# Performance work log

Measured on AMD Instinct MI355X. Metric: run time of the kernel, lower is better.

The kernel has to match this reference:

```python
import jax, jax.numpy as jnp
import numpy as np

B, L, IN, H, T = 512, 16, 128, 1024, 64


def setup_inputs() -> dict:
    key = jax.random.key(0)
    ks = jax.random.split(key, 11)
    k = 1.0 / np.sqrt(H)  # torch default init scale
    u = lambda kk, shape: jax.random.uniform(kk, shape, jnp.float32, -k, k)
    return {
        "x": jax.random.normal(ks[0], (B, L, IN), jnp.float32),
        "W_ih0": u(ks[1], (4 * H, IN)),
        "W_hh0": u(ks[2], (4 * H, H)),
        "b_ih0": u(ks[3], (4 * H,)),
        "b_hh0": u(ks[4], (4 * H,)),
        "W_ih1": u(ks[5], (4 * H, H)),
        "W_hh1": u(ks[6], (4 * H, H)),
        "b_ih1": u(ks[7], (4 * H,)),
        "b_hh1": u(ks[8], (4 * H,)),
        "W_out": u(ks[9], (IN, H)),
        "b_out": u(ks[10], (IN,)),
        "t": T,
    }


def _cell(xt, h, c, W_ih, W_hh, b_ih, b_hh):
    # PyTorch LSTM cell; gate order i, f, g, o
    g = xt @ W_ih.T + h @ W_hh.T + (b_ih + b_hh)
    i, f, gg, o = jnp.split(g, 4, axis=-1)
    c = jax.nn.sigmoid(f) * c + jax.nn.sigmoid(i) * jnp.tanh(gg)
    h = jax.nn.sigmoid(o) * jnp.tanh(c)
    return h, c


def reference(x, W_ih0, W_hh0, b_ih0, b_hh0, W_ih1, W_hh1, b_ih1, b_hh1,
              W_out, b_out, t):
    layers = ((W_ih0, W_hh0, b_ih0, b_hh0), (W_ih1, W_hh1, b_ih1, b_hh1))
    Bn = x.shape[0]
    Hn = W_hh0.shape[1]

    def stack_step(state, xt):
        new_state = []
        inp = xt
        for (h, c), p in zip(state, layers):
            h, c = _cell(inp, h, c, *p)
            new_state.append((h, c))
            inp = h
        return tuple(new_state), inp  # inp = top-layer hidden [B, H]

    z = jnp.zeros((Bn, Hn), x.dtype)
    state0 = tuple((z, z) for _ in layers)

    # prompt phase: process x over time, keep final state and last top hidden
    state, tops = jax.lax.scan(stack_step, state0, x.transpose(1, 0, 2))
    x_last = x[:, -1] + (tops[-1] @ W_out.T + b_out)  # [B, IN]

    def gen_step(carry, _):
        st, xl = carry
        st, htop = stack_step(st, xl)
        xl = xl + (htop @ W_out.T + b_out)
        return (st, xl), xl

    (_, _), gen = jax.lax.scan(gen_step, (state, x_last), None, length=t - 1)

    out = jnp.concatenate(
        [x, x_last[:, None, :], gen.transpose(1, 0, 2)], axis=1
    )  # [B, L + t, IN]
    return out
```

## Files before the change

### kernel.cpp

```cpp
#include <hip/hip_runtime.h>

#define B_    512
#define L_    16
#define IN_   128
#define H_    1024
#define T_    64
#define OUTROW 10240

#define LDC   1040
#define LDXL  144
#define RSTRIDE 67
#define RSZ   (64 * RSTRIDE)

#define KH_X  64
#define KH_H  32
#define KH_XL 4
#define KH_W0 36
#define KH_W1 64
#define KH_WO 32

typedef __attribute__((ext_vector_type(8))) short bf8;
typedef __attribute__((ext_vector_type(4))) float f4;
typedef __attribute__((ext_vector_type(4))) unsigned short us4;
typedef unsigned short u16;
typedef unsigned int   u32;

#define MFMA16(a, b, c) __builtin_amdgcn_mfma_f32_16x16x32_bf16(a, b, c, 0, 0, 0)

__device__ __forceinline__ u16 f2bf(float f) {
    u32 u = __builtin_bit_cast(u32, f);
    u32 r = (u + 0x7fffu + ((u >> 16) & 1u)) >> 16;
    return (u16)r;
}
__device__ __forceinline__ float sigm(float x) { return 1.f / (1.f + __expf(-x)); }
__device__ __forceinline__ float tanh_f(float x) {
    float ax = fabsf(x);
    float e = __expf(-2.f * ax);
    float t = (1.f - e) / (1.f + e);
    return x < 0.f ? -t : t;
}
__device__ __forceinline__ bf8 ld8(const u16* p) { return *(const bf8*)p; }

__device__ __forceinline__ size_t swz(int kh_stride, int row, int k) {
    return ((size_t)(row >> 4) * kh_stride + (k >> 5)) * 512
           + ((k & 31) >> 3) * 128 + (row & 15) * 8 + (k & 7);
}

#define MFMAP(AS, BS)                                                       \
  do {                                                                      \
    _Pragma("unroll")                                                       \
    for (int g_ = 0; g_ < 4; ++g_)                                          \
      _Pragma("unroll")                                                     \
      for (int t_ = 0; t_ < 4; ++t_)                                        \
        acc[g_][t_] = MFMA16(AS[g_], BS[t_], acc[g_][t_]);                  \
  } while (0)

#define LOADP_CELL(AS, BS, PH)                                              \
  do {                                                                      \
    const int kt_ = ws + (((PH) >> 1) << 2);                                \
    const int s_  = (PH) & 1;                                               \
    const bool ix_ = kt_ < nk1;                                             \
    const int oA_ = (((ix_ ? kt_ : kt_ - nk1) << 1) + s_) * 512;            \
    const int oB_ = ((kt_ << 1) + s_) * 512;                                \
    _Pragma("unroll")                                                       \
    for (int g_ = 0; g_ < 4; ++g_)                                          \
      AS[g_] = ld8((ix_ ? apx[g_] : aph[g_]) + oA_);                        \
    _Pragma("unroll")                                                       \
    for (int t_ = 0; t_ < 4; ++t_) BS[t_] = ld8(bp[t_] + oB_);              \
  } while (0)

__device__ __forceinline__ void cell_body(int bid,
    const u16* __restrict__ pA0, int kh0, int nk1,
    const u16* __restrict__ pA1, int kh1, int nk2,
    const u16* __restrict__ pB, int khB,
    const float* __restrict__ bias, float* __restrict__ Cst,
    u16* __restrict__ Hdst, float* __restrict__ red)
{
    const int tn = (bid & 7) * 8 + ((bid >> 3) & 7);
    const int tm = bid >> 6;
    const int tid = threadIdx.x;
    const int lane = tid & 63, ws = tid >> 6;
    const int l15 = lane & 15, qd = lane >> 4, q4 = qd * 4;

    const int erow = ws * 16 + l15;
    const int grow = tm * 64 + erow;
    const int colb = tn * 16 + q4;
    const f4 cold = *(const f4*)&Cst[(size_t)grow * LDC + colb];

    f4 acc[4][4];
#pragma unroll
    for (int i = 0; i < 4; ++i)
#pragma unroll
        for (int j = 0; j < 4; ++j) acc[i][j] = (f4)(0.f);

    const u16* bp[4];
#pragma unroll
    for (int t = 0; t < 4; ++t)
        bp[t] = pB + (size_t)(tn * 4 + t) * khB * 512 + lane * 8;
    const u16* apx[4];
    const u16* aph[4];
#pragma unroll
    for (int g = 0; g < 4; ++g) {
        apx[g] = pA0 + (size_t)(tm * 4 + g) * kh0 * 512 + lane * 8;
        aph[g] = pA1 + (size_t)(tm * 4 + g) * kh1 * 512 + lane * 8;
    }

    const int nk  = nk1 + nk2;
    const int myn = (nk - ws + 3) >> 2;
    const int nph = myn * 2;

    bf8 A0[4], B0[4], A1[4], B1[4], A2[4], B2[4], A3[4], B3[4];
    LOADP_CELL(A0, B0, 0);
    LOADP_CELL(A1, B1, 1);
    LOADP_CELL(A2, B2, 2);
    int ph = 0;
    for (; ph + 4 <= nph; ph += 4) {
        LOADP_CELL(A3, B3, ph + 3);
        MFMAP(A0, B0);
        if (ph + 4 < nph) LOADP_CELL(A0, B0, ph + 4);
        MFMAP(A1, B1);
        if (ph + 5 < nph) LOADP_CELL(A1, B1, ph + 5);
        MFMAP(A2, B2);
        if (ph + 6 < nph) LOADP_CELL(A2, B2, ph + 6);
        MFMAP(A3, B3);
    }
    if (ph < nph) {
        MFMAP(A0, B0);
        MFMAP(A1, B1);
    }

#pragma unroll
    for (int rg = 0; rg < 4; ++rg)
#pragma unroll
        for (int t = 0; t < 4; ++t)
#pragma unroll
            for (int r = 0; r < 4; ++r)
                red[ws * RSZ + (rg * 16 + q4 + r) * RSTRIDE + t * 16 + l15] = acc[rg][t][r];
    __syncthreads();

    f4 gs[4];
#pragma unroll
    for (int G = 0; G < 4; ++G) {
        f4 s;
#pragma unroll
        for (int j = 0; j < 4; ++j) {
            const int cidx = erow * RSTRIDE + G * 16 + q4 + j;
            s[j] = red[0 * RSZ + cidx] + red[1 * RSZ + cidx]
                 + red[2 * RSZ + cidx] + red[3 * RSZ + cidx];
        }
        gs[G] = s + *(const f4*)&bias[tn * 64 + G * 16 + q4];
    }
    f4 cn; us4 h4;
#pragma unroll
    for (int j = 0; j < 4; ++j) {
        const float I  = sigm(gs[0][j]);
        const float F  = sigm(gs[1][j]);
        const float Gg = tanh_f(gs[2][j]);
        const float O  = sigm(gs[3][j]);
        cn[j] = F * cold[j] + I * Gg;
        h4[j] = f2bf(O * tanh_f(cn[j]));
    }
    *(f4*)&Cst[(size_t)grow * LDC + colb] = cn;
    *(us4*)&Hdst[swz(KH_H, grow, colb)] = h4;
}

__global__ __launch_bounds__(256, 2) void cell_gemm(
    const u16* __restrict__ pA0, int kh0, int nk1,
    const u16* __restrict__ pA1, int kh1, int nk2,
    const u16* __restrict__ pB, int khB,
    const float* __restrict__ bias, float* __restrict__ Cst, u16* __restrict__ Hdst)
{
    __shared__ float red[4 * RSZ];
    cell_body(blockIdx.x, pA0, kh0, nk1, pA1, kh1, nk2, pB, khB, bias, Cst, Hdst, red);
}

__global__ __launch_bounds__(256, 2) void pair_k(
    const u16* __restrict__ A0a, int kh0a, int nk1a,
    const u16* __restrict__ A1a, int kh1a, int nk2a,
    const u16* __restrict__ Ba, int khBa,
    const float* __restrict__ ba, float* __restrict__ Ca, u16* __restrict__ Ha,
    const u16* __restrict__ A0b, int kh0b, int nk1b,
    const u16* __restrict__ A1b, int kh1b, int nk2b,
    const u16* __restrict__ Bb, int khBb,
    const float* __restrict__ bb, float* __restrict__ Cb, u16* __restrict__ Hb)
{
    __shared__ float red[4 * RSZ];
    if (blockIdx.x < 512)
        cell_body(blockIdx.x, A0a, kh0a, nk1a, A1a, kh1a, nk2a, Ba, khBa, ba, Ca, Ha, red);
    else
        cell_body(blockIdx.x - 512, A0b, kh0b, nk1b, A1b, kh1b, nk2b, Bb, khBb, bb, Cb, Hb, red);
}

__global__ __launch_bounds__(256, 2) void proj64_k(
    const u16* __restrict__ pH1, const u16* __restrict__ pWo,
    const float* __restrict__ bout_,
    const float* __restrict__ xin, int ldxin,
    float* __restrict__ XL, u16* __restrict__ XLbf,
    float* __restrict__ dout, int slot)
{
    __shared__ float red[4 * RSZ];
    const int pb = blockIdx.x;
    const int tm = pb >> 3, cg = pb & 7;
    const int tid = threadIdx.x;
    const int lane = tid & 63, ws = tid >> 6;
    const int l15 = lane & 15, qd = lane >> 4;

    const u16* ap[4];
#pragma unroll
    for (int g = 0; g < 4; ++g)
        ap[g] = pH1 + (size_t)(tm * 4 + g) * (KH_H * 512) + lane * 8;
    const u16* bp = pWo + (size_t)cg * (KH_WO * 512) + lane * 8;

    f4 acc[4];
#pragma unroll
    for (int g = 0; g < 4; ++g) acc[g] = (f4)(0.f);

    for (int m = 0; m < 4; ++m) {
#pragma unroll
        for (int sh = 0; sh < 2; ++sh) {
            const int o = (((ws + m * 4) << 1) + sh) * 512;
            const bf8 Bv = ld8(bp + o);
#pragma unroll
            for (int g = 0; g < 4; ++g)
                acc[g] = MFMA16(ld8(ap[g] + o), Bv, acc[g]);
        }
    }

#pragma unroll
    for (int g = 0; g < 4; ++g)
#pragma unroll
        for (int r = 0; r < 4; ++r)
            red[ws * RSZ + (g * 16 + qd * 4 + r) * RSTRIDE + l15] = acc[g][r];
    __syncthreads();

    const int row = tid >> 2, c4 = (tid & 3) * 4;
    const int col = cg * 16 + c4;
    const int grow = tm * 64 + row;
    f4 s;
#pragma unroll
    for (int j = 0; j < 4; ++j) {
        const int cidx = row * RSTRIDE + c4 + j;
        s[j] = red[0 * RSZ + cidx] + red[1 * RSZ + cidx]
             + red[2 * RSZ + cidx] + red[3 * RSZ + cidx];
    }
    const f4 v = *(const f4*)&xin[(size_t)grow * ldxin + col] + s
                 + *(const f4*)&bout_[col];
    *(f4*)&XL[(size_t)grow * LDXL + col] = v;
    us4 b;
#pragma unroll
    for (int j = 0; j < 4; ++j) b[j] = f2bf(v[j]);
    *(us4*)&XLbf[swz(KH_XL, grow, col)] = b;
    *(f4*)&dout[(size_t)grow * OUTROW + slot * IN_ + col] = v;
}

__global__ void conv_w(const float* Wih0, const float* Whh0, const float* bih0, const float* bhh0,
                       const float* Wih1, const float* Whh1, const float* bih1, const float* bhh1,
                       const float* Wout,
                       u16* W0c, float* b0p, u16* W1c, float* b1p, u16* Woutb)
{
    const int bid = blockIdx.x, t = threadIdx.x;
    const int lane = t >> 2;
    const int l15 = lane & 15, qd = lane >> 4;
    const int j0 = (t & 3) * 2;
    const int c0_ = qd * 8 + j0;

    if (bid < 9216) {
        const int rg = bid / 36, kh = bid - rg * 36;
        const int p = rg * 16 + l15;
        const int rem = p & 63, G = rem >> 4, u = (p >> 6) * 16 + (rem & 15);
        const int src = G * H_ + u;
        float e0, e1;
        if (kh < 4) {
            e0 = Wih0[(size_t)src * IN_ + kh * 32 + c0_];
            e1 = Wih0[(size_t)src * IN_ + kh * 32 + c0_ + 1];
        } else {
            e0 = Whh0[(size_t)src * H_ + (kh - 4) * 32 + c0_];
            e1 = Whh0[(size_t)src * H_ + (kh - 4) * 32 + c0_ + 1];
        }
        ((u32*)W0c)[(size_t)bid * 256 + t] = (u32)f2bf(e0) | ((u32)f2bf(e1) << 16);
        if (kh == 0 && qd == 0 && j0 == 0) b0p[p] = bih0[src] + bhh0[src];
    } else if (bid < 25600) {
        const int x = bid - 9216;
        const int rg = x >> 6, kh = x & 63;
        const int p = rg * 16 + l15;
        const int rem = p & 63, G = rem >> 4, u = (p >> 6) * 16 + (rem & 15);
        const int src = G * H_ + u;
        float e0, e1;
        if (kh < 32) {
            e0 = Wih1[(size_t)src * H_ + kh * 32 + c0_];
            e1 = Wih1[(size_t)src * H_ + kh * 32 + c0_ + 1];
        } else {
            e0 = Whh1[(size_t)src * H_ + (kh - 32) * 32 + c0_];
            e1 = Whh1[(size_t)src * H_ + (kh - 32) * 32 + c0_ + 1];
        }
        ((u32*)W1c)[(size_t)x * 256 + t] = (u32)f2bf(e0) | ((u32)f2bf(e1) << 16);
        if (kh == 0 && qd == 0 && j0 == 0) b1p[p] = bih1[src] + bhh1[src];
    } else {
        const int x = bid - 25600;
        const int rg = x >> 5, kh = x & 31;
        const int r = rg * 16 + l15;
        const float e0 = Wout[(size_t)r * H_ + kh * 32 + c0_];
        const float e1 = Wout[(size_t)r * H_ + kh * 32 + c0_ + 1];
        ((u32*)Woutb)[(size_t)x * 256 + t] = (u32)f2bf(e0) | ((u32)f2bf(e1) << 16);
    }
}

__global__ void setup_k(const float* __restrict__ x, u16* __restrict__ Xb,
                        u16* H0, u16* H1, float* c0, float* c1,
                        float* __restrict__ dout)
{
    const int i = blockIdx.x * 256 + threadIdx.x;
    const float v = x[i];
    const int r = i >> 11, col = i & 2047;
    Xb[swz(KH_X, r, col)] = f2bf(v);
    dout[(size_t)r * OUTROW + col] = v;
    if (i < B_ * H_) {
        H0[i] = 0; H1[i] = 0;
        const int rr = i >> 10, cc = i & 1023;
        c0[(size_t)rr * LDC + cc] = 0.f; c1[(size_t)rr * LDC + cc] = 0.f;
    }
}

extern "C" void kernel_launch(void* const* d_in, const int* in_sizes, int n_in,
                              void* d_out, int out_size, void* d_ws, size_t ws_size,
                              hipStream_t stream)
{
    const float* x    = (const float*)d_in[0];
    const float* Wih0 = (const float*)d_in[1];
    const float* Whh0 = (const float*)d_in[2];
    const float* bih0 = (const float*)d_in[3];
    const float* bhh0 = (const float*)d_in[4];
    const float* Wih1 = (const float*)d_in[5];
    const float* Whh1 = (const float*)d_in[6];
    const float* bih1 = (const float*)d_in[7];
    const float* bhh1 = (const float*)d_in[8];
    const float* Wout = (const float*)d_in[9];
    const float* bout = (const float*)d_in[10];
    float* dout = (float*)d_out;

    char* ws = (char*)d_ws;
    size_t off = 0;
    auto alloc = [&](size_t bytes) -> char* {
        char* p = ws + off; off += (bytes + 255) & ~(size_t)255; return p;
    };
    u16*  W0c   = (u16*)alloc((size_t)9216 * 1024);
    u16*  W1c   = (u16*)alloc((size_t)16384 * 1024);
    u16*  Woutb = (u16*)alloc((size_t)256 * 1024);
    float* b0p  = (float*)alloc(4096 * 4);
    float* b1p  = (float*)alloc(4096 * 4);
    u16*  Xb    = (u16*)alloc((size_t)2048 * 1024);
    u16*  H0b[2]; H0b[0] = (u16*)alloc((size_t)1024 * 1024); H0b[1] = (u16*)alloc((size_t)1024 * 1024);
    u16*  H1b[2]; H1b[0] = (u16*)alloc((size_t)1024 * 1024); H1b[1] = (u16*)alloc((size_t)1024 * 1024);
    float* c0   = (float*)alloc((size_t)B_ * LDC * 4);
    float* c1   = (float*)alloc((size_t)B_ * LDC * 4);
    float* XL   = (float*)alloc((size_t)B_ * LDXL * 4);
    u16*  XLbf  = (u16*)alloc((size_t)128 * 1024);

    conv_w<<<25856, 256, 0, stream>>>(Wih0, Whh0, bih0, bhh0,
                                      Wih1, Whh1, bih1, bhh1, Wout,
                                      W0c, b0p, W1c, b1p, Woutb);
    setup_k<<<4096, 256, 0, stream>>>(x, Xb, H0b[0], H1b[0], c0, c1, dout);

    int p = 0;
    cell_gemm<<<512, 256, 0, stream>>>(Xb, KH_X, 2, H0b[0], KH_H, 16,
                                       W0c, KH_W0, b0p, c0, H0b[1]);
    for (int g = 0; g < 15; ++g) {
        pair_k<<<1024, 256, 0, stream>>>(
            H0b[1 - p], KH_H, 16, H1b[p], KH_H, 16, W1c, KH_W1, b1p, c1, H1b[1 - p],
            Xb + (size_t)(g + 1) * 2048, KH_X, 2, H0b[1 - p], KH_H, 16,
            W0c, KH_W0, b0p, c0, H0b[p]);
        p ^= 1;
    }
    cell_gemm<<<512, 256, 0, stream>>>(H0b[0], KH_H, 16, H1b[1], KH_H, 16,
                                       W1c, KH_W1, b1p, c1, H1b[0]);
    proj64_k<<<64, 256, 0, stream>>>(H1b[0], Woutb, bout,
                                     x + 15 * IN_, L_ * IN_, XL, XLbf, dout, 16);

    p = 0;
    for (int g = 16; g < 79; ++g) {
        cell_gemm<<<512, 256, 0, stream>>>(XLbf, KH_XL, 2, H0b[p], KH_H, 16,
                                           W0c, KH_W0, b0p, c0, H0b[1 - p]);
        cell_gemm<<<512, 256, 0, stream>>>(H0b[1 - p], KH_H, 16, H1b[p], KH_H, 16,
                                           W1c, KH_W1, b1p, c1, H1b[1 - p]);
        const int s = g - 15;
        proj64_k<<<64, 256, 0, stream>>>(H1b[1 - p], Woutb, bout,
                                         XL, LDXL, XL, XLbf, dout, 16 + s);
        p ^= 1;
    }
}
```

Baseline: 2.413 ms.

## Fuse output projection into next layer-0 cell kernel with flag-based intra-grid sync

Merges the per-step output projection (proj64_k) into the following layer-0 cell GEMM kernel. The first 64 blocks compute the projection and publish XL via cache-bypassing stores, then bump a global counter. All blocks do the recurrent H-part of the GEMM first and spin on the counter before consuming the new input. This removes one kernel launch per generation step and overlaps the projection with the recurrent GEMM. In exchange it relies on all 64 producer blocks being co-resident or scheduled first, and it adds spin-wait and coherence overhead.

```diff
diff --git a/kernel.cpp b/kernel.cpp
--- a/kernel.cpp
+++ b/kernel.cpp
@@ -40,6 +40,17 @@
     return x < 0.f ? -t : t;
 }
 __device__ __forceinline__ bf8 ld8(const u16* p) { return *(const bf8*)p; }
+
+__device__ __forceinline__ bf8 ld8_cc(const u16* p) {
+    bf8 r;
+    asm volatile("global_load_dwordx4 %0, %1, off sc0 sc1"
+                 : "=v"(r) : "v"(p) : "memory");
+    return r;
+}
+__device__ __forceinline__ void st8_cc(u16* p, us4 v) {
+    asm volatile("global_store_dwordx2 %0, %1, off sc0 sc1"
+                 :: "v"(p), "v"(v) : "memory");
+}
 
 __device__ __forceinline__ size_t swz(int kh_stride, int row, int k) {
     return ((size_t)(row >> 4) * kh_stride + (k >> 5)) * 512
@@ -251,6 +262,182 @@
     for (int j = 0; j < 4; ++j) b[j] = f2bf(v[j]);
     *(us4*)&XLbf[swz(KH_XL, grow, col)] = b;
     *(f4*)&dout[(size_t)grow * OUTROW + slot * IN_ + col] = v;
+}
+
+__global__ __launch_bounds__(256, 2) void fuse0_k(
+    const u16* __restrict__ pH1, const u16* __restrict__ pWo,
+    const float* __restrict__ bout_,
+    const float* __restrict__ xin, int ldxin,
+    float* __restrict__ XL, u16* __restrict__ XLbf,
+    float* __restrict__ dout, int slot,
+    const u16* __restrict__ pH0, const u16* __restrict__ pW0,
+    const float* __restrict__ bias, float* __restrict__ Cst,
+    u16* __restrict__ Hdst, u32* flag, u32 target)
+{
+    __shared__ float red[4 * RSZ];
+    const int bid = blockIdx.x;
+    const int tid = threadIdx.x;
+    const int lane = tid & 63, ws = tid >> 6;
+    const int l15 = lane & 15, qd = lane >> 4, q4 = qd * 4;
+
+    const int tn = (bid & 7) * 8 + ((bid >> 3) & 7);
+    const int tm = bid >> 6;
+    const int erow = ws * 16 + l15;
+    const int grow = tm * 64 + erow;
+    const int colb = tn * 16 + q4;
+    const f4 cold = *(const f4*)&Cst[(size_t)grow * LDC + colb];
+
+    if (bid < 64) {
+        const int ptm = bid >> 3, cg = bid & 7;
+        const u16* ap[4];
+#pragma unroll
+        for (int g = 0; g < 4; ++g)
+            ap[g] = pH1 + (size_t)(ptm * 4 + g) * (KH_H * 512) + lane * 8;
+        const u16* pbp = pWo + (size_t)cg * (KH_WO * 512) + lane * 8;
+
+        f4 pacc[4];
+#pragma unroll
+        for (int g = 0; g < 4; ++g) pacc[g] = (f4)(0.f);
+        for (int m = 0; m < 4; ++m) {
+#pragma unroll
+            for (int sh = 0; sh < 2; ++sh) {
+                const int o = (((ws + m * 4) << 1) + sh) * 512;
+                const bf8 Bv = ld8(pbp + o);
+#pragma unroll
+                for (int g = 0; g < 4; ++g)
+                    pacc[g] = MFMA16(ld8(ap[g] + o), Bv, pacc[g]);
+            }
+        }
+#pragma unroll
+        for (int g = 0; g < 4; ++g)
+#pragma unroll
+            for (int r = 0; r < 4; ++r)
+                red[ws * RSZ + (g * 16 + qd * 4 + r) * RSTRIDE + l15] = pacc[g][r];
+        __syncthreads();
+
+        const int prow = tid >> 2, c4 = (tid & 3) * 4;
+        const int col = cg * 16 + c4;
+        const int pgrow = ptm * 64 + prow;
+        f4 s;
+#pragma unroll
+        for (int j = 0; j < 4; ++j) {
+            const int cidx = prow * RSTRIDE + c4 + j;
+            s[j] = red[0 * RSZ + cidx] + red[1 * RSZ + cidx]
+                 + red[2 * RSZ + cidx] + red[3 * RSZ + cidx];
+        }
+        const f4 v = *(const f4*)&xin[(size_t)pgrow * ldxin + col] + s
+                     + *(const f4*)&bout_[col];
+        *(f4*)&XL[(size_t)pgrow * LDXL + col] = v;
+        *(f4*)&dout[(size_t)pgrow * OUTROW + slot * IN_ + col] = v;
+        us4 b;
+#pragma unroll
+        for (int j = 0; j < 4; ++j) b[j] = f2bf(v[j]);
+        st8_cc(&XLbf[swz(KH_XL, pgrow, col)], b);
+        asm volatile("s_waitcnt vmcnt(0)" ::: "memory");
+        __syncthreads();
+        if (tid == 0)
+            __hip_atomic_fetch_add(flag, 1u, __ATOMIC_RELAXED,
+                                   __HIP_MEMORY_SCOPE_AGENT);
+    }
+
+    f4 acc[4][4];
+#pragma unroll
+    for (int i = 0; i < 4; ++i)
+#pragma unroll
+        for (int j = 0; j < 4; ++j) acc[i][j] = (f4)(0.f);
+
+    const u16* bp[4];
+#pragma unroll
+    for (int t = 0; t < 4; ++t)
+        bp[t] = pW0 + (size_t)(tn * 4 + t) * (KH_W0 * 512) + lane * 8;
+    const u16* ah[4];
+#pragma unroll
+    for (int g = 0; g < 4; ++g)
+        ah[g] = pH0 + (size_t)(tm * 4 + g) * (KH_H * 512) + lane * 8;
+
+    const int j0 = (ws < 2) ? ws + 2 : ws - 2;
+
+#define LOADH(AS, BS, Q)                                                    \
+  do {                                                                      \
+    const int j_ = j0 + ((((Q) >> 1)) << 2);                                \
+    const int oA_ = (2 * j_ + ((Q) & 1)) * 512;                             \
+    _Pragma("unroll")                                                       \
+    for (int g_ = 0; g_ < 4; ++g_) AS[g_] = ld8(ah[g_] + oA_);              \
+    _Pragma("unroll")                                                       \
+    for (int t_ = 0; t_ < 4; ++t_) BS[t_] = ld8(bp[t_] + oA_ + 4 * 512);    \
+  } while (0)
+
+    {
+        bf8 A0[4], B0[4], A1[4], B1[4];
+        LOADH(A0, B0, 0);
+        for (int q = 0; q < 8; q += 2) {
+            LOADH(A1, B1, q + 1);
+            MFMAP(A0, B0);
+            if (q + 2 < 8) LOADH(A0, B0, q + 2);
+            MFMAP(A1, B1);
+        }
+    }
+#undef LOADH
+
+    if (ws < 2) {
+        while (__hip_atomic_load(flag, __ATOMIC_RELAXED,
+                                 __HIP_MEMORY_SCOPE_AGENT) < target)
+            __builtin_amdgcn_s_sleep(4);
+        const u16* xp[4];
+#pragma unroll
+        for (int g = 0; g < 4; ++g)
+            xp[g] = XLbf + (size_t)(tm * 4 + g) * (KH_XL * 512) + lane * 8;
+        bf8 XA[2][4], XB[2][4];
+#pragma unroll
+        for (int sh = 0; sh < 2; ++sh) {
+            const int o = (2 * ws + sh) * 512;
+#pragma unroll
+            for (int g = 0; g < 4; ++g) XA[sh][g] = ld8_cc(xp[g] + o);
+#pragma unroll
+            for (int t = 0; t < 4; ++t) XB[sh][t] = ld8(bp[t] + o);
+        }
+        asm volatile("s_waitcnt vmcnt(0)"
+                     : "+v"(XA[0][0]), "+v"(XA[0][1]), "+v"(XA[0][2]), "+v"(XA[0][3]),
+                       "+v"(XA[1][0]), "+v"(XA[1][1]), "+v"(XA[1][2]), "+v"(XA[1][3]) ::);
+        __builtin_amdgcn_sched_barrier(0);
+#pragma unroll
+        for (int sh = 0; sh < 2; ++sh) MFMAP(XA[sh], XB[sh]);
+    }
+
+    __syncthreads();
+#pragma unroll
+    for (int rg = 0; rg < 4; ++rg)
+#pragma unroll
+        for (int t = 0; t < 4; ++t)
+#pragma unroll
+            for (int r = 0; r < 4; ++r)
+                red[ws * RSZ + (rg * 16 + q4 + r) * RSTRIDE + t * 16 + l15] = acc[rg][t][r];
+    __syncthreads();
+
+    f4 gs[4];
+#pragma unroll
+    for (int G = 0; G < 4; ++G) {
+        f4 s;
+#pragma unroll
+        for (int j = 0; j < 4; ++j) {
+            const int cidx = erow * RSTRIDE + G * 16 + q4 + j;
+            s[j] = red[0 * RSZ + cidx] + red[1 * RSZ + cidx]
+                 + red[2 * RSZ + cidx] + red[3 * RSZ + cidx];
+        }
+        gs[G] = s + *(const f4*)&bias[tn * 64 + G * 16 + q4];
+    }
+    f4 cn; us4 h4;
+#pragma unroll
+    for (int j = 0; j < 4; ++j) {
+        const float I  = sigm(gs[0][j]);
+        const float F  = sigm(gs[1][j]);
+        const float Gg = tanh_f(gs[2][j]);
+        const float O  = sigm(gs[3][j]);
+        cn[j] = F * cold[j] + I * Gg;
+        h4[j] = f2bf(O * tanh_f(cn[j]));
+    }
+    *(f4*)&Cst[(size_t)grow * LDC + colb] = cn;
+    *(us4*)&Hdst[swz(KH_H, grow, colb)] = h4;
 }
 
 __global__ void conv_w(const float* Wih0, const float* Whh0, const float* bih0, const float* bhh0,
@@ -307,9 +494,10 @@
 
 __global__ void setup_k(const float* __restrict__ x, u16* __restrict__ Xb,
                         u16* H0, u16* H1, float* c0, float* c1,
-                        float* __restrict__ dout)
+                        float* __restrict__ dout, u32* flag)
 {
     const int i = blockIdx.x * 256 + threadIdx.x;
+    if (i < 64) flag[i] = 0;
     const float v = x[i];
     const int r = i >> 11, col = i & 2047;
     Xb[swz(KH_X, r, col)] = f2bf(v);
@@ -355,11 +543,12 @@
     float* c1   = (float*)alloc((size_t)B_ * LDC * 4);
     float* XL   = (float*)alloc((size_t)B_ * LDXL * 4);
     u16*  XLbf  = (u16*)alloc((size_t)128 * 1024);
+    u32*  flag  = (u32*)alloc(256 * 4);
 
     conv_w<<<25856, 256, 0, stream>>>(Wih0, Whh0, bih0, bhh0,
                                       Wih1, Whh1, bih1, bhh1, Wout,
                                       W0c, b0p, W1c, b1p, Woutb);
-    setup_k<<<4096, 256, 0, stream>>>(x, Xb, H0b[0], H1b[0], c0, c1, dout);
+    setup_k<<<4096, 256, 0, stream>>>(x, Xb, H0b[0], H1b[0], c0, c1, dout, flag);
 
     int p = 0;
     cell_gemm<<<512, 256, 0, stream>>>(Xb, KH_X, 2, H0b[0], KH_H, 16,
@@ -373,18 +562,20 @@
     }
     cell_gemm<<<512, 256, 0, stream>>>(H0b[0], KH_H, 16, H1b[1], KH_H, 16,
                                        W1c, KH_W1, b1p, c1, H1b[0]);
-    proj64_k<<<64, 256, 0, stream>>>(H1b[0], Woutb, bout,
-                                     x + 15 * IN_, L_ * IN_, XL, XLbf, dout, 16);
 
     p = 0;
-    for (int g = 16; g < 79; ++g) {
-        cell_gemm<<<512, 256, 0, stream>>>(XLbf, KH_XL, 2, H0b[p], KH_H, 16,
-                                           W0c, KH_W0, b0p, c0, H0b[1 - p]);
+    for (int e = 0; e < 63; ++e) {
+        const float* xin; int ldxin;
+        if (e == 0) { xin = x + 15 * IN_; ldxin = L_ * IN_; }
+        else        { xin = XL;           ldxin = LDXL;     }
+        fuse0_k<<<512, 256, 0, stream>>>(H1b[p], Woutb, bout, xin, ldxin,
+                                         XL, XLbf, dout, 16 + e,
+                                         H0b[p], W0c, b0p, c0, H0b[1 - p],
+                                         flag, 64u * (u32)(e + 1));
         cell_gemm<<<512, 256, 0, stream>>>(H0b[1 - p], KH_H, 16, H1b[p], KH_H, 16,
                                            W1c, KH_W1, b1p, c1, H1b[1 - p]);
-        const int s = g - 15;
-        proj64_k<<<64, 256, 0, stream>>>(H1b[1 - p], Woutb, bout,
-                                         XL, LDXL, XL, XLbf, dout, 16 + s);
         p ^= 1;
     }
-}
+    proj64_k<<<64, 256, 0, stream>>>(H1b[1], Woutb, bout,
+                                     XL, LDXL, XL, XLbf, dout, 79);
+}
```

Result: faster. 2.346 ms (-2.8%).
